# Optimization experiments

Measured on AMD Instinct MI355X. Metric: run time of the kernel, lower is better.

The kernel has to match this reference:

```python
import jax, jax.numpy as jnp
import numpy as np

N = 40000      # nodes
E = 640000     # edges
R = 4          # relations (n_edge_features)
F = 128        # n_node_features
H = 128        # n_hidden
NB = 2         # num_convolution_blocks
G = 64         # graphs in batch
OUT = 10       # n_output
MAXDEG = 10    # PyG MFConv default max_degree


def setup_inputs() -> dict:
    key = jax.random.key(0)
    ks = jax.random.split(key, 20)
    s = 0.05
    return {
        "x": jax.random.normal(ks[0], (N, F), dtype=jnp.float32),
        "edge_index": jax.random.randint(ks[1], (2, E), 0, N, dtype=jnp.int32),
        "edge_attr": jax.random.randint(ks[2], (E,), 0, R, dtype=jnp.int32),
        "batch_idx": jnp.sort(jax.random.randint(ks[3], (N,), 0, G, dtype=jnp.int32)),
        # node embedding Linear(F -> H)
        "W0": jax.random.normal(ks[4], (F, H), dtype=jnp.float32) * s,
        "b0": jnp.zeros((H,), dtype=jnp.float32),
        # per-block RGCNConv params (stacked over blocks)
        "rgcn_Wrel": jax.random.normal(ks[5], (NB, R, H, H), dtype=jnp.float32) * s,
        "rgcn_Wroot": jax.random.normal(ks[6], (NB, H, H), dtype=jnp.float32) * s,
        "rgcn_b": jnp.zeros((NB, H), dtype=jnp.float32),
        # per-block MFConv params: lins_l (bias) and lins_r (no bias), one per degree 0..MAXDEG
        "mf_Wl": jax.random.normal(ks[7], (NB, MAXDEG + 1, H, H), dtype=jnp.float32) * s,
        "mf_bl": jnp.zeros((NB, MAXDEG + 1, H), dtype=jnp.float32),
        "mf_Wr": jax.random.normal(ks[8], (NB, MAXDEG + 1, H, H), dtype=jnp.float32) * s,
        # after-pool MLP
        "W1": jax.random.normal(ks[9], (H, H), dtype=jnp.float32) * s,
        "b1": jnp.zeros((H,), dtype=jnp.float32),
        "W2": jax.random.normal(ks[10], (H, OUT), dtype=jnp.float32) * s,
        "b2": jnp.zeros((OUT,), dtype=jnp.float32),
    }


def _rgcn(h, Wrel, Wroot, b, src, dst, etype):
    # PyG RGCNConv: per-relation mean of neighbor features, then relation GEMM, plus root + bias
    n = h.shape[0]
    idx = dst * R + etype                                   # fused (node, relation) segment id
    msg = h[src]                                            # [E, H] gather
    sums = jax.ops.segment_sum(msg, idx, num_segments=n * R).reshape(n, R, -1)
    cnt = jax.ops.segment_sum(jnp.ones((msg.shape[0],), h.dtype), idx,
                              num_segments=n * R).reshape(n, R, 1)
    mean = jnp.where(cnt > 0, sums / jnp.maximum(cnt, 1.0), 0.0)
    return jnp.einsum('nrh,rho->no', mean, Wrel) + h @ Wroot + b


def _mfconv(h, Wl, bl, Wr, src, dst, deg):
    # PyG MFConv: sum-aggregate neighbors, then degree-specific lin_l(agg) + lin_r(x)
    n = h.shape[0]
    agg = jax.ops.segment_sum(h[src], dst, num_segments=n)  # [N, H]
    out = jnp.zeros((n, Wl.shape[-1]), h.dtype)
    for d in range(MAXDEG + 1):                             # small fixed loop over degree buckets
        m = (deg == d).astype(h.dtype)[:, None]
        out = out + m * (agg @ Wl[d] + bl[d] + h @ Wr[d])
    return out


def reference(x, edge_index, edge_attr, batch_idx,
              W0, b0, rgcn_Wrel, rgcn_Wroot, rgcn_b,
              mf_Wl, mf_bl, mf_Wr, W1, b1, W2, b2):
    src, dst = edge_index[0], edge_index[1]
    etype = edge_attr
    n = x.shape[0]
    # node degree at targets (all relations), clamped to MAXDEG (PyG MFConv)
    deg = jnp.clip(jax.ops.segment_sum(jnp.ones((src.shape[0],), jnp.int32), dst,
                                       num_segments=n), 0, MAXDEG)
    h = x @ W0 + b0
    for blk in range(NB):
        h = jax.nn.relu(h)
        h = _rgcn(h, rgcn_Wrel[blk], rgcn_Wroot[blk], rgcn_b[blk], src, dst, etype)
        h = jax.nn.relu(h)
        h = _mfconv(h, mf_Wl[blk], mf_bl[blk], mf_Wr[blk], src, dst, deg)
    pooled = jax.ops.segment_sum(h, batch_idx, num_segments=G)  # global add pool [G, H]
    out = jax.nn.relu(pooled @ W1 + b1) @ W2 + b2
    return out
```

## Files before the change

kernel.cpp:

```cpp
#include <hip/hip_runtime.h>
#include <hip/hip_bf16.h>

#define N_NODES 40000
#define N_EDGES 640000
#define R_REL 4
#define F_IN 128
#define H_DIM 128
#define NBLK 2
#define G_GRAPHS 64
#define N_OUT 10
#define MAXDEG 10
#define NSCAN_BLK ((N_NODES + 255) / 256)

typedef unsigned short u16;
typedef float f32x4 __attribute__((ext_vector_type(4)));
typedef short bf16x8 __attribute__((ext_vector_type(8)));

__device__ __forceinline__ float relu_f(float x){ return x > 0.f ? x : 0.f; }

__device__ __forceinline__ u16 f2bf(float f){
  union { float f; unsigned int u; } v; v.f = f;
  unsigned int r = v.u + 0x7fffu + ((v.u >> 16) & 1u);
  return (u16)(r >> 16);
}
__device__ __forceinline__ float b2f(u16 u){
  union { unsigned int u; float f; } v; v.u = ((unsigned int)u) << 16; return v.f;
}
__device__ __forceinline__ float blo(unsigned v){ return b2f((u16)v); }
__device__ __forceinline__ float bhi(unsigned v){ return b2f((u16)(v >> 16)); }

__device__ __forceinline__ void gload16(const void* g, void* l){
  __builtin_amdgcn_global_load_lds(
      (const __attribute__((address_space(1))) void*)g,
      (__attribute__((address_space(3))) void*)l, 16, 0, 0);
}

__device__ __forceinline__ void unpk8(uint4 v, float* f){
  f[0] = blo(v.x); f[1] = bhi(v.x);
  f[2] = blo(v.y); f[3] = bhi(v.y);
  f[4] = blo(v.z); f[5] = bhi(v.z);
  f[6] = blo(v.w); f[7] = bhi(v.w);
}

__global__ void k_cnt(const int* __restrict__ dst, const int* __restrict__ et, int* __restrict__ cnt4){
  int e = blockIdx.x * blockDim.x + threadIdx.x;
  if (e >= N_EDGES) return;
  atomicAdd(&cnt4[dst[e] * R_REL + et[e]], 1);
}

__global__ __launch_bounds__(256) void k_scan_a(const int* __restrict__ cnt4, int* __restrict__ deg,
                                                int* __restrict__ row_ptr, int* __restrict__ bsum,
                                                int* __restrict__ bhist){
  __shared__ int s[256];
  __shared__ int lh[16];
  int tid = threadIdx.x;
  int i = blockIdx.x * 256 + tid;
  if (tid < 16) lh[tid] = 0;
  int d = 0;
  if (i < N_NODES){
    int4 c = *(const int4*)(cnt4 + (size_t)i * 4);
    d = c.x + c.y + c.z + c.w;
    deg[i] = d;
  }
  s[tid] = d;
  __syncthreads();
  if (i < N_NODES){
    int dc = d > MAXDEG ? MAXDEG : d;
    atomicAdd(&lh[dc], 1);
  }
  for (int o = 1; o < 256; o <<= 1){
    int t = (tid >= o) ? s[tid - o] : 0;
    __syncthreads();
    s[tid] += t;
    __syncthreads();
  }
  if (i < N_NODES) row_ptr[i] = s[tid] - d;
  if (tid == 255) bsum[blockIdx.x] = s[255];
  if (tid <= MAXDEG) bhist[blockIdx.x * (MAXDEG + 1) + tid] = lh[tid];
}

__global__ __launch_bounds__(256) void k_scan_bb(int* __restrict__ bsum, int* __restrict__ bbase,
                                                 const int* __restrict__ bhist, int* __restrict__ pbase,
                                                 int* __restrict__ bcount, int* __restrict__ boff){
  __shared__ int s[256];
  __shared__ int cnt_s[MAXDEG + 1];
  __shared__ int off_s[MAXDEG + 1];
  int tid = threadIdx.x;
  int v = (tid < NSCAN_BLK) ? bsum[tid] : 0;
  s[tid] = v;
  __syncthreads();
  for (int o = 1; o < 256; o <<= 1){
    int t = (tid >= o) ? s[tid - o] : 0;
    __syncthreads();
    s[tid] += t;
    __syncthreads();
  }
  if (tid < NSCAN_BLK) bbase[tid] = s[tid] - v;

  if (tid <= MAXDEG){
    int run = 0;
    for (int b = 0; b < NSCAN_BLK; ++b){
      pbase[b * (MAXDEG + 1) + tid] = run;
      run += bhist[b * (MAXDEG + 1) + tid];
    }
    cnt_s[tid] = run;
    bcount[tid] = run;
  }
  __syncthreads();
  if (tid == 0){
    int acc = 0;
    for (int dd = 0; dd <= MAXDEG; ++dd){ off_s[dd] = acc; boff[dd] = acc; acc += cnt_s[dd]; }
  }
  __syncthreads();
  if (tid <= MAXDEG){
    int base = off_s[tid];
    for (int b = 0; b < NSCAN_BLK; ++b) pbase[b * (MAXDEG + 1) + tid] += base;
  }
}

__global__ __launch_bounds__(256) void k_scan_c(int* __restrict__ row_ptr, const int* __restrict__ bbase,
                                                const int* __restrict__ cnt4, int* __restrict__ rel_off,
                                                int* __restrict__ cursor){
  int i = blockIdx.x * 256 + threadIdx.x;
  if (i < N_NODES){
    int base = row_ptr[i] + bbase[blockIdx.x];
    row_ptr[i] = base;
    int4 c = *(const int4*)(cnt4 + (size_t)i * 4);
    int4 o;
    o.x = base;
    o.y = base + c.x;
    o.z = o.y + c.y;
    o.w = o.z + c.z;
    *(int4*)(rel_off + (size_t)i * 4) = o;
    *(int4*)(cursor + (size_t)i * 4) = o;
  }
  if (i == 0) row_ptr[N_NODES] = N_EDGES;
}

__global__ void k_csr_fill(const int* __restrict__ src, const int* __restrict__ dst,
                           const int* __restrict__ et,
                           int* __restrict__ cursor, int* __restrict__ esrc){
  int e = blockIdx.x * blockDim.x + threadIdx.x;
  if (e >= N_EDGES) return;
  int cell = dst[e] * R_REL + et[e];
  int p = atomicAdd(&cursor[cell], 1);
  esrc[p] = src[e];
}

__global__ __launch_bounds__(256) void k_bfill(const int* __restrict__ deg, const int* __restrict__ pbase,
                                               int* __restrict__ perm){
  __shared__ int lh[MAXDEG + 1];
  int tid = threadIdx.x;
  if (tid <= MAXDEG) lh[tid] = 0;
  __syncthreads();
  int i = blockIdx.x * 256 + tid;
  if (i < N_NODES){
    int d = deg[i]; if (d > MAXDEG) d = MAXDEG;
    int lpos = atomicAdd(&lh[d], 1);
    perm[pbase[blockIdx.x * (MAXDEG + 1) + d] + lpos] = i;
  }
}

__global__ __launch_bounds__(256) void k_cvtW_all(const float* __restrict__ s0, const float* __restrict__ s1,
                                                  const float* __restrict__ s2, const float* __restrict__ s3,
                                                  const float* __restrict__ s4,
                                                  u16* __restrict__ d0, u16* __restrict__ d1,
                                                  u16* __restrict__ d2, u16* __restrict__ d3,
                                                  u16* __restrict__ d4){
  __shared__ float s[32][33];
  int b = blockIdx.x;
  int m = b >> 4, tile = b & 15;
  const float* S; u16* D; int base;
  if (m < 1){ S = s0; D = d0; base = m; }
  else if (m < 9){ S = s1; D = d1; base = m - 1; }
  else if (m < 11){ S = s2; D = d2; base = m - 9; }
  else if (m < 33){ S = s3; D = d3; base = m - 11; }
  else { S = s4; D = d4; base = m - 33; }
  S += (size_t)base * 16384;
  D += (size_t)base * 16384;
  int tr = (tile >> 2) * 32, tc = (tile & 3) * 32;
  int c = threadIdx.x & 31, r0 = threadIdx.x >> 5;
  #pragma unroll
  for (int i = 0; i < 4; ++i){
    int r = r0 + i * 8;
    s[r][c] = S[(size_t)(tr + r) * 128 + tc + c];
  }
  __syncthreads();
  #pragma unroll
  for (int i = 0; i < 4; ++i){
    int r = r0 + i * 8;
    D[(size_t)(tc + r) * 128 + tr + c] = f2bf(s[c][r]);
  }
}

__global__ void k_cvtx(const float* __restrict__ x, u16* __restrict__ xb){
  int t = blockIdx.x * 256 + threadIdx.x;
  if (t >= (N_NODES * H_DIM) / 4) return;
  float4 v = ((const float4*)x)[t];
  uint2 o = make_uint2((unsigned)f2bf(v.x) | ((unsigned)f2bf(v.y) << 16),
                       (unsigned)f2bf(v.z) | ((unsigned)f2bf(v.w) << 16));
  ((uint2*)xb)[t] = o;
}

__global__ __launch_bounds__(256) void k_rgcn_agg(const u16* __restrict__ hb,
                                                  const int* __restrict__ rel_off,
                                                  const int* __restrict__ row_ptr,
                                                  const int* __restrict__ esrc,
                                                  u16* __restrict__ meanb){
  int node = blockIdx.x * 4 + (threadIdx.x >> 6);
  int lane = threadIdx.x & 63;
  int g = lane >> 4, c = lane & 15;
  int4 ro = *(const int4*)(rel_off + (size_t)node * 4);
  int nend = row_ptr[node + 1];
  int beg_g = (g == 0) ? ro.x : (g == 1) ? ro.y : (g == 2) ? ro.z : ro.w;
  int end_g = (g == 0) ? ro.y : (g == 1) ? ro.z : (g == 2) ? ro.w : nend;
  float acc[8];
  #pragma unroll
  for (int j = 0; j < 8; ++j) acc[j] = 0.f;
  const u16* hc = hb + c * 8;

  int e = beg_g;
  for (; e + 2 <= end_g; e += 2){
    int s0 = esrc[e], s1 = esrc[e + 1];
    uint4 v0 = *(const uint4*)(hc + (size_t)s0 * H_DIM);
    uint4 v1 = *(const uint4*)(hc + (size_t)s1 * H_DIM);
    float f0[8], f1[8];
    unpk8(v0, f0); unpk8(v1, f1);
    #pragma unroll
    for (int j = 0; j < 8; ++j) acc[j] += f0[j] + f1[j];
  }
  if (e < end_g){
    uint4 v0 = *(const uint4*)(hc + (size_t)esrc[e] * H_DIM);
    float f0[8];
    unpk8(v0, f0);
    #pragma unroll
    for (int j = 0; j < 8; ++j) acc[j] += f0[j];
  }
  int cnt = end_g - beg_g;
  float inv = cnt > 0 ? 1.f / (float)cnt : 0.f;
  unsigned p[4];
  #pragma unroll
  for (int q = 0; q < 4; ++q)
    p[q] = (unsigned)f2bf(acc[q * 2] * inv) | ((unsigned)f2bf(acc[q * 2 + 1] * inv) << 16);
  *(uint4*)(meanb + (size_t)node * R_REL * H_DIM + g * H_DIM + c * 8) =
      make_uint4(p[0], p[1], p[2], p[3]);
}

__global__ __launch_bounds__(256) void k_mf_agg(const u16* __restrict__ hb,
                                                const int* __restrict__ row_ptr,
                                                const int* __restrict__ esrc,
                                                u16* __restrict__ aggb){
  int node = blockIdx.x * 4 + (threadIdx.x >> 6);
  int lane = threadIdx.x & 63;
  int g = lane >> 4, c = lane & 15;
  int beg = row_ptr[node], end = row_ptr[node + 1];
  int T = end - beg;
  float acc[8];
  #pragma unroll
  for (int j = 0; j < 8; ++j) acc[j] = 0.f;
  const u16* hc = hb + c * 8;

  int i = 0;
  for (; i + 8 <= T; i += 8){
    int eA = beg + i + g, eB = beg + i + 4 + g;
    int sA = esrc[eA], sB = esrc[eB];
    uint4 vA = *(const uint4*)(hc + (size_t)sA * H_DIM);
    uint4 vB = *(const uint4*)(hc + (size_t)sB * H_DIM);
    float fA[8], fB[8];
    unpk8(vA, fA); unpk8(vB, fB);
    #pragma unroll
    for (int j = 0; j < 8; ++j) acc[j] += fA[j] + fB[j];
  }
  for (; i < T; i += 4){
    int e = beg + i + g;
    int ce = e < end ? e : end - 1;
    int s = esrc[ce];
    uint4 v = *(const uint4*)(hc + (size_t)s * H_DIM);
    float f[8];
    unpk8(v, f);
    float m = (e < end) ? 1.f : 0.f;
    #pragma unroll
    for (int j = 0; j < 8; ++j) acc[j] += f[j] * m;
  }
  #pragma unroll
  for (int j = 0; j < 8; ++j){
    acc[j] += __shfl_xor(acc[j], 16, 64);
    acc[j] += __shfl_xor(acc[j], 32, 64);
  }
  if (g == 0){
    unsigned p[4];
    #pragma unroll
    for (int q = 0; q < 4; ++q)
      p[q] = (unsigned)f2bf(acc[q * 2]) | ((unsigned)f2bf(acc[q * 2 + 1]) << 16);
    uint4 P = make_uint4(p[0], p[1], p[2], p[3]);
    *(uint4*)(aggb + (size_t)node * H_DIM + c * 8) = P;
  }
}


__global__ __launch_bounds__(512) void k_gemm0(const u16* __restrict__ xb, const u16* __restrict__ wt,
                                               const float* __restrict__ bias, u16* __restrict__ hbo){
  __shared__ u16 lds[32][128];
  int tid = threadIdx.x;
  int w = tid >> 6, lane = tid & 63;
  int m0 = blockIdx.x * 32;
  int rg = lane >> 4, cb = (lane & 15) << 4;
  int srow = w * 4 + rg;
  int swcb = cb ^ ((srow & 7) << 4);
  gload16(xb + (size_t)(m0 + srow) * F_IN + (swcb >> 1), &lds[w * 4][0]);
  __syncthreads();

  int arow = lane & 15, kg = lane >> 4;
  int col = w * 16 + arow;
  f32x4 acc[2];
  acc[0] = (f32x4){0.f, 0.f, 0.f, 0.f};
  acc[1] = (f32x4){0.f, 0.f, 0.f, 0.f};
  bf16x8 b[4];
  #pragma unroll
  for (int kk = 0; kk < 4; ++kk)
    b[kk] = *(const bf16x8*)(wt + (size_t)col * F_IN + kk * 32 + kg * 8);
  #pragma unroll
  for (int rt = 0; rt < 2; ++rt){
    int row = rt * 16 + arow;
    const char* base = (const char*)&lds[0][0] + row * 256;
    int sx = (row & 7) << 4;
    #pragma unroll
    for (int kk = 0; kk < 4; ++kk){
      bf16x8 a = *(const bf16x8*)(base + ((kk * 64 + kg * 16) ^ sx));
      acc[rt] = __builtin_amdgcn_mfma_f32_16x16x32_bf16(a, b[kk], acc[rt], 0, 0, 0);
    }
  }
  float bb = bias[col];
  #pragma unroll
  for (int rt = 0; rt < 2; ++rt)
    #pragma unroll
    for (int j = 0; j < 4; ++j){
      int gr = m0 + rt * 16 + kg * 4 + j;
      hbo[(size_t)gr * H_DIM + col] = f2bf(relu_f(acc[rt][j] + bb));
    }
}

__global__ __launch_bounds__(512) void k_rgcn_gemm(const u16* __restrict__ meanb, const u16* __restrict__ hb,
                                                   const u16* __restrict__ wrel, const u16* __restrict__ wroot,
                                                   const float* __restrict__ bias, u16* __restrict__ hbo){
  __shared__ u16 lds[5][32][128];
  int tid = threadIdx.x;
  int w = tid >> 6, lane = tid & 63;
  int m0 = blockIdx.x * 32;
  int rg = lane >> 4, cb = (lane & 15) << 4;
  int srow = w * 4 + rg;
  int swcb = cb ^ ((srow & 7) << 4);
  #pragma unroll
  for (int s = 0; s < 4; ++s)
    gload16(meanb + ((size_t)(m0 + srow) * R_REL + s) * H_DIM + (swcb >> 1), &lds[s][w * 4][0]);
  gload16(hb + (size_t)(m0 + srow) * H_DIM + (swcb >> 1), &lds[4][w * 4][0]);
  __syncthreads();

  int arow = lane & 15, kg = lane >> 4;
  int col = w * 16 + arow;
  f32x4 acc[2];
  acc[0] = (f32x4){0.f, 0.f, 0.f, 0.f};
  acc[1] = (f32x4){0.f, 0.f, 0.f, 0.f};
  #pragma unroll
  for (int s = 0; s < 5; ++s){
    const u16* WT = (s < 4) ? wrel + (size_t)s * 16384 : wroot;
    bf16x8 b[4];
    #pragma unroll
    for (int kk = 0; kk < 4; ++kk)
      b[kk] = *(const bf16x8*)(WT + (size_t)col * H_DIM + kk * 32 + kg * 8);
    #pragma unroll
    for (int rt = 0; rt < 2; ++rt){
      int row = rt * 16 + arow;
      const char* base = (const char*)&lds[s][0][0] + row * 256;
      int sx = (row & 7) << 4;
      #pragma unroll
      for (int kk = 0; kk < 4; ++kk){
        bf16x8 a = *(const bf16x8*)(base + ((kk * 64 + kg * 16) ^ sx));
        acc[rt] = __builtin_amdgcn_mfma_f32_16x16x32_bf16(a, b[kk], acc[rt], 0, 0, 0);
      }
    }
  }
  float bb = bias[col];
  #pragma unroll
  for (int rt = 0; rt < 2; ++rt)
    #pragma unroll
    for (int j = 0; j < 4; ++j){
      int gr = m0 + rt * 16 + kg * 4 + j;
      hbo[(size_t)gr * H_DIM + col] = f2bf(relu_f(acc[rt][j] + bb));
    }
}

template<int FINAL>
__global__ __launch_bounds__(512) void k_mf_gemm(const u16* __restrict__ aggb, const u16* __restrict__ hb,
                                                 const u16* __restrict__ wl, const u16* __restrict__ wr,
                                                 const float* __restrict__ bl,
                                                 const int* __restrict__ bcount, const int* __restrict__ boff,
                                                 const int* __restrict__ perm,
                                                 u16* __restrict__ hbo, float* __restrict__ hf){
  __shared__ u16 lds[2][32][128];
  __shared__ int rows_s[32];
  int t = blockIdx.x;
  int d = -1, tile = 0;
  for (int dd = 0; dd <= MAXDEG; ++dd){
    int nt = (bcount[dd] + 31) >> 5;
    if (t < nt){ d = dd; tile = t; break; }
    t -= nt;
  }
  if (d < 0) return;
  int cnt_d = bcount[d];
  int start = boff[d] + tile * 32;
  int nrows = cnt_d - tile * 32; if (nrows > 32) nrows = 32;

  int tid = threadIdx.x;
  int w = tid >> 6, lane = tid & 63;
  if (tid < 32) rows_s[tid] = (tid < nrows) ? perm[start + tid] : -1;

  int rg = lane >> 4, cb = (lane & 15) << 4;
  int srow = w * 4 + rg;
  int swcb = cb ^ ((srow & 7) << 4);
  int node = perm[start + (srow < nrows ? srow : 0)];
  gload16(aggb + (size_t)node * H_DIM + (swcb >> 1), &lds[0][w * 4][0]);
  gload16(hb   + (size_t)node * H_DIM + (swcb >> 1), &lds[1][w * 4][0]);
  __syncthreads();

  int arow = lane & 15, kg = lane >> 4;
  int col = w * 16 + arow;
  f32x4 acc[2];
  acc[0] = (f32x4){0.f, 0.f, 0.f, 0.f};
  acc[1] = (f32x4){0.f, 0.f, 0.f, 0.f};
  #pragma unroll
  for (int s = 0; s < 2; ++s){
    const u16* WT = (s ? wr : wl) + (size_t)d * 16384;
    bf16x8 b[4];
    #pragma unroll
    for (int kk = 0; kk < 4; ++kk)
      b[kk] = *(const bf16x8*)(WT + (size_t)col * H_DIM + kk * 32 + kg * 8);
    #pragma unroll
    for (int rt = 0; rt < 2; ++rt){
      int row = rt * 16 + arow;
      const char* base = (const char*)&lds[s][0][0] + row * 256;
      int sx = (row & 7) << 4;
      #pragma unroll
      for (int kk = 0; kk < 4; ++kk){
        bf16x8 a = *(const bf16x8*)(base + ((kk * 64 + kg * 16) ^ sx));
        acc[rt] = __builtin_amdgcn_mfma_f32_16x16x32_bf16(a, b[kk], acc[rt], 0, 0, 0);
      }
    }
  }
  float bb = bl[(size_t)d * H_DIM + col];
  #pragma unroll
  for (int rt = 0; rt < 2; ++rt)
    #pragma unroll
    for (int j = 0; j < 4; ++j){
      int gr = rows_s[rt * 16 + kg * 4 + j];
      if (gr >= 0){
        float v = acc[rt][j] + bb;
        if (FINAL) hf[(size_t)gr * H_DIM + col] = v;
        else       hbo[(size_t)gr * H_DIM + col] = f2bf(relu_f(v));
      }
    }
}

__global__ void k_goff(const int* __restrict__ batch, int* __restrict__ goff){
  int n = blockIdx.x * blockDim.x + threadIdx.x;
  if (n >= N_NODES) return;
  int b = batch[n];
  int bp = (n == 0) ? -1 : batch[n - 1];
  for (int g = bp + 1; g <= b; ++g) goff[g] = n;
  if (n == N_NODES - 1){
    for (int g = b + 1; g <= G_GRAPHS; ++g) goff[g] = N_NODES;
  }
}

__global__ __launch_bounds__(256) void k_pool(const float* __restrict__ h, const int* __restrict__ goff,
                                              float* __restrict__ pooled){
  __shared__ float4 sred[8][32];
  int g = blockIdx.x;
  int tid = threadIdx.x;
  int rg = tid >> 5, lane = tid & 31;
  int beg = goff[g], end = goff[g + 1];
  float4 acc = make_float4(0.f, 0.f, 0.f, 0.f);
  for (int n = beg + rg; n < end; n += 8){
    float4 v = ((const float4*)(h + (size_t)n * H_DIM))[lane];
    acc.x += v.x; acc.y += v.y; acc.z += v.z; acc.w += v.w;
  }
  sred[rg][lane] = acc;
  __syncthreads();
  if (tid < 32){
    float4 s = sred[0][tid];
    #pragma unroll
    for (int r = 1; r < 8; ++r){
      float4 v = sred[r][tid];
      s.x += v.x; s.y += v.y; s.z += v.z; s.w += v.w;
    }
    *(float4*)(pooled + (size_t)g * H_DIM + tid * 4) = s;
  }
}

__global__ __launch_bounds__(128) void k_mlp(const float* __restrict__ pooled,
                                             const float* __restrict__ W1, const float* __restrict__ b1,
                                             const float* __restrict__ W2, const float* __restrict__ b2,
                                             float* __restrict__ out){
  __shared__ float Ts[128];
  int g = blockIdx.x, j = threadIdx.x;
  const float* p = pooled + (size_t)g * H_DIM;
  float s = b1[j];
  for (int k = 0; k < H_DIM; ++k) s += p[k] * W1[k * H_DIM + j];
  Ts[j] = relu_f(s);
  __syncthreads();
  if (j < N_OUT){
    float o = b2[j];
    for (int k = 0; k < H_DIM; ++k) o += Ts[k] * W2[k * N_OUT + j];
    out[(size_t)g * N_OUT + j] = o;
  }
}

extern "C" void kernel_launch(void* const* d_in, const int* in_sizes, int n_in,
                              void* d_out, int out_size, void* d_ws, size_t ws_size,
                              hipStream_t stream){
  const float* x      = (const float*)d_in[0];
  const int*   ei     = (const int*)d_in[1];
  const int*   ea     = (const int*)d_in[2];
  const int*   batch  = (const int*)d_in[3];
  const float* W0     = (const float*)d_in[4];
  const float* b0     = (const float*)d_in[5];
  const float* rWrel  = (const float*)d_in[6];
  const float* rWroot = (const float*)d_in[7];
  const float* rb     = (const float*)d_in[8];
  const float* mWl    = (const float*)d_in[9];
  const float* mbl    = (const float*)d_in[10];
  const float* mWr    = (const float*)d_in[11];
  const float* W1     = (const float*)d_in[12];
  const float* b1     = (const float*)d_in[13];
  const float* W2     = (const float*)d_in[14];
  const float* b2     = (const float*)d_in[15];
  float* out = (float*)d_out;

  const int* src = ei;
  const int* dst = ei + N_EDGES;

  char* ws = (char*)d_ws;
  size_t off = 0;
  auto alloc = [&](size_t bytes) -> void* {
    void* p = ws + off;
    off += (bytes + 255) & ~(size_t)255;
    return p;
  };
  u16* xb      = (u16*)alloc((size_t)N_NODES * H_DIM * 2);
  u16* hbA     = (u16*)alloc((size_t)N_NODES * H_DIM * 2);
  u16* hbB     = (u16*)alloc((size_t)N_NODES * H_DIM * 2);
  u16* meanb   = (u16*)alloc((size_t)N_NODES * R_REL * H_DIM * 2);
  u16* aggb    = meanb;
  float* hf    = (float*)alloc((size_t)N_NODES * H_DIM * 4);
  u16* wt0     = (u16*)alloc((size_t)1 * 16384 * 2);
  u16* wtRel   = (u16*)alloc((size_t)NBLK * R_REL * 16384 * 2);
  u16* wtRoot  = (u16*)alloc((size_t)NBLK * 16384 * 2);
  u16* wtWl    = (u16*)alloc((size_t)NBLK * (MAXDEG + 1) * 16384 * 2);
  u16* wtWr    = (u16*)alloc((size_t)NBLK * (MAXDEG + 1) * 16384 * 2);
  float* pooled = (float*)alloc((size_t)G_GRAPHS * H_DIM * 4);
  int* cnt4     = (int*)alloc((size_t)N_NODES * R_REL * 4);
  int* deg      = (int*)alloc((size_t)N_NODES * 4);
  int* row_ptr  = (int*)alloc((size_t)(N_NODES + 1) * 4);
  int* rel_off  = (int*)alloc((size_t)N_NODES * R_REL * 4);
  int* cursor   = (int*)alloc((size_t)N_NODES * R_REL * 4);
  int* esrc     = (int*)alloc((size_t)N_EDGES * 4);
  int* bsum     = (int*)alloc((size_t)NSCAN_BLK * 4);
  int* bbase    = (int*)alloc((size_t)NSCAN_BLK * 4);
  int* bhist    = (int*)alloc((size_t)NSCAN_BLK * (MAXDEG + 1) * 4);
  int* pbase    = (int*)alloc((size_t)NSCAN_BLK * (MAXDEG + 1) * 4);
  int* perm     = (int*)alloc((size_t)N_NODES * 4);
  int* bcount   = (int*)alloc(16 * 4);
  int* boff     = (int*)alloc(16 * 4);
  int* goff     = (int*)alloc((size_t)(G_GRAPHS + 1) * 4);

  hipMemsetAsync(cnt4, 0, (size_t)N_NODES * R_REL * 4, stream);

  k_cnt<<<(N_EDGES + 255) / 256, 256, 0, stream>>>(dst, ea, cnt4);
  k_scan_a<<<NSCAN_BLK, 256, 0, stream>>>(cnt4, deg, row_ptr, bsum, bhist);
  k_scan_bb<<<1, 256, 0, stream>>>(bsum, bbase, bhist, pbase, bcount, boff);
  k_scan_c<<<NSCAN_BLK, 256, 0, stream>>>(row_ptr, bbase, cnt4, rel_off, cursor);
  k_csr_fill<<<(N_EDGES + 255) / 256, 256, 0, stream>>>(src, dst, ea, cursor, esrc);
  k_bfill<<<NSCAN_BLK, 256, 0, stream>>>(deg, pbase, perm);
  k_goff<<<(N_NODES + 255) / 256, 256, 0, stream>>>(batch, goff);

  k_cvtW_all<<<55 * 16, 256, 0, stream>>>(W0, rWrel, rWroot, mWl, mWr,
                                          wt0, wtRel, wtRoot, wtWl, wtWr);
  k_cvtx<<<(N_NODES * H_DIM / 4 + 255) / 256, 256, 0, stream>>>(x, xb);

  k_gemm0<<<N_NODES / 32, 512, 0, stream>>>(xb, wt0, b0, hbA);

  u16* hin = hbA;
  u16* hout = hbB;
  for (int blk = 0; blk < NBLK; ++blk){
    k_rgcn_agg<<<N_NODES / 4, 256, 0, stream>>>(hin, rel_off, row_ptr, esrc, meanb);
    k_rgcn_gemm<<<N_NODES / 32, 512, 0, stream>>>(meanb, hin,
        wtRel + (size_t)blk * R_REL * 16384,
        wtRoot + (size_t)blk * 16384,
        rb + (size_t)blk * H_DIM, hout);
    { u16* tmp = hin; hin = hout; hout = tmp; }

    k_mf_agg<<<N_NODES / 4, 256, 0, stream>>>(hin, row_ptr, esrc, aggb);
    const u16* wl_b = wtWl + (size_t)blk * (MAXDEG + 1) * 16384;
    const u16* wr_b = wtWr + (size_t)blk * (MAXDEG + 1) * 16384;
    const float* bl_b = mbl + (size_t)blk * (MAXDEG + 1) * H_DIM;
    int grid_mf = N_NODES / 32 + MAXDEG + 1;
    if (blk == NBLK - 1)
      k_mf_gemm<1><<<grid_mf, 512, 0, stream>>>(aggb, hin, wl_b, wr_b, bl_b,
                                                bcount, boff, perm, hout, hf);
    else
      k_mf_gemm<0><<<grid_mf, 512, 0, stream>>>(aggb, hin, wl_b, wr_b, bl_b,
                                                bcount, boff, perm, hout, hf);
    { u16* tmp = hin; hin = hout; hout = tmp; }
  }

  k_pool<<<G_GRAPHS, 256, 0, stream>>>(hf, goff, pooled);
  k_mlp<<<G_GRAPHS, 128, 0, stream>>>(pooled, W1, b1, W2, b2, out);
}
```

Baseline: 359.3 us.

## Fuse x conversion into gemm0, merge goff/bfill and pool/mlp, unroll rgcn gather

```diff
diff --git a/kernel.cpp b/kernel.cpp
--- a/kernel.cpp
+++ b/kernel.cpp
@@ -147,8 +147,9 @@
   esrc[p] = src[e];
 }
 
-__global__ __launch_bounds__(256) void k_bfill(const int* __restrict__ deg, const int* __restrict__ pbase,
-                                               int* __restrict__ perm){
+__global__ __launch_bounds__(256) void k_bfill_goff(const int* __restrict__ deg, const int* __restrict__ pbase,
+                                                    int* __restrict__ perm,
+                                                    const int* __restrict__ batch, int* __restrict__ goff){
   __shared__ int lh[MAXDEG + 1];
   int tid = threadIdx.x;
   if (tid <= MAXDEG) lh[tid] = 0;
@@ -158,6 +159,13 @@
     int d = deg[i]; if (d > MAXDEG) d = MAXDEG;
     int lpos = atomicAdd(&lh[d], 1);
     perm[pbase[blockIdx.x * (MAXDEG + 1) + d] + lpos] = i;
+
+    int b = batch[i];
+    int bp = (i == 0) ? -1 : batch[i - 1];
+    for (int g = bp + 1; g <= b; ++g) goff[g] = i;
+    if (i == N_NODES - 1){
+      for (int g = b + 1; g <= G_GRAPHS; ++g) goff[g] = N_NODES;
+    }
   }
 }
 
@@ -193,15 +201,6 @@
   }
 }
 
-__global__ void k_cvtx(const float* __restrict__ x, u16* __restrict__ xb){
-  int t = blockIdx.x * 256 + threadIdx.x;
-  if (t >= (N_NODES * H_DIM) / 4) return;
-  float4 v = ((const float4*)x)[t];
-  uint2 o = make_uint2((unsigned)f2bf(v.x) | ((unsigned)f2bf(v.y) << 16),
-                       (unsigned)f2bf(v.z) | ((unsigned)f2bf(v.w) << 16));
-  ((uint2*)xb)[t] = o;
-}
-
 __global__ __launch_bounds__(256) void k_rgcn_agg(const u16* __restrict__ hb,
                                                   const int* __restrict__ rel_off,
                                                   const int* __restrict__ row_ptr,
@@ -220,6 +219,17 @@
   const u16* hc = hb + c * 8;
 
   int e = beg_g;
+  for (; e + 4 <= end_g; e += 4){
+    int s0 = esrc[e], s1 = esrc[e + 1], s2 = esrc[e + 2], s3 = esrc[e + 3];
+    uint4 v0 = *(const uint4*)(hc + (size_t)s0 * H_DIM);
+    uint4 v1 = *(const uint4*)(hc + (size_t)s1 * H_DIM);
+    uint4 v2 = *(const uint4*)(hc + (size_t)s2 * H_DIM);
+    uint4 v3 = *(const uint4*)(hc + (size_t)s3 * H_DIM);
+    float f0[8], f1[8], f2[8], f3[8];
+    unpk8(v0, f0); unpk8(v1, f1); unpk8(v2, f2); unpk8(v3, f3);
+    #pragma unroll
+    for (int j = 0; j < 8; ++j) acc[j] += (f0[j] + f1[j]) + (f2[j] + f3[j]);
+  }
   for (; e + 2 <= end_g; e += 2){
     int s0 = esrc[e], s1 = esrc[e + 1];
     uint4 v0 = *(const uint4*)(hc + (size_t)s0 * H_DIM);
@@ -298,16 +308,25 @@
 }
 
 
-__global__ __launch_bounds__(512) void k_gemm0(const u16* __restrict__ xb, const u16* __restrict__ wt,
+__global__ __launch_bounds__(512) void k_gemm0(const float* __restrict__ x, const u16* __restrict__ wt,
                                                const float* __restrict__ bias, u16* __restrict__ hbo){
   __shared__ u16 lds[32][128];
   int tid = threadIdx.x;
   int w = tid >> 6, lane = tid & 63;
   int m0 = blockIdx.x * 32;
-  int rg = lane >> 4, cb = (lane & 15) << 4;
-  int srow = w * 4 + rg;
-  int swcb = cb ^ ((srow & 7) << 4);
-  gload16(xb + (size_t)(m0 + srow) * F_IN + (swcb >> 1), &lds[w * 4][0]);
+  {
+    int rg = lane >> 4, cb = (lane & 15) << 4;
+    int srow = w * 4 + rg;
+    int swcb = cb ^ ((srow & 7) << 4);
+    const float* xs = x + (size_t)(m0 + srow) * F_IN + (swcb >> 1);
+    float4 u = *(const float4*)xs;
+    float4 v = *(const float4*)(xs + 4);
+    unsigned p0 = (unsigned)f2bf(u.x) | ((unsigned)f2bf(u.y) << 16);
+    unsigned p1 = (unsigned)f2bf(u.z) | ((unsigned)f2bf(u.w) << 16);
+    unsigned p2 = (unsigned)f2bf(v.x) | ((unsigned)f2bf(v.y) << 16);
+    unsigned p3 = (unsigned)f2bf(v.z) | ((unsigned)f2bf(v.w) << 16);
+    *(uint4*)((char*)&lds[0][0] + w * 1024 + lane * 16) = make_uint4(p0, p1, p2, p3);
+  }
   __syncthreads();
 
   int arow = lane & 15, kg = lane >> 4;
@@ -461,20 +480,13 @@
     }
 }
 
-__global__ void k_goff(const int* __restrict__ batch, int* __restrict__ goff){
-  int n = blockIdx.x * blockDim.x + threadIdx.x;
-  if (n >= N_NODES) return;
-  int b = batch[n];
-  int bp = (n == 0) ? -1 : batch[n - 1];
-  for (int g = bp + 1; g <= b; ++g) goff[g] = n;
-  if (n == N_NODES - 1){
-    for (int g = b + 1; g <= G_GRAPHS; ++g) goff[g] = N_NODES;
-  }
-}
-
-__global__ __launch_bounds__(256) void k_pool(const float* __restrict__ h, const int* __restrict__ goff,
-                                              float* __restrict__ pooled){
+__global__ __launch_bounds__(256) void k_poolmlp(const float* __restrict__ h, const int* __restrict__ goff,
+                                                 const float* __restrict__ W1, const float* __restrict__ b1,
+                                                 const float* __restrict__ W2, const float* __restrict__ b2,
+                                                 float* __restrict__ out){
   __shared__ float4 sred[8][32];
+  __shared__ float pv[128];
+  __shared__ float Ts[128];
   int g = blockIdx.x;
   int tid = threadIdx.x;
   int rg = tid >> 5, lane = tid & 31;
@@ -493,25 +505,19 @@
       float4 v = sred[r][tid];
       s.x += v.x; s.y += v.y; s.z += v.z; s.w += v.w;
     }
-    *(float4*)(pooled + (size_t)g * H_DIM + tid * 4) = s;
-  }
-}
-
-__global__ __launch_bounds__(128) void k_mlp(const float* __restrict__ pooled,
-                                             const float* __restrict__ W1, const float* __restrict__ b1,
-                                             const float* __restrict__ W2, const float* __restrict__ b2,
-                                             float* __restrict__ out){
-  __shared__ float Ts[128];
-  int g = blockIdx.x, j = threadIdx.x;
-  const float* p = pooled + (size_t)g * H_DIM;
-  float s = b1[j];
-  for (int k = 0; k < H_DIM; ++k) s += p[k] * W1[k * H_DIM + j];
-  Ts[j] = relu_f(s);
-  __syncthreads();
-  if (j < N_OUT){
-    float o = b2[j];
-    for (int k = 0; k < H_DIM; ++k) o += Ts[k] * W2[k * N_OUT + j];
-    out[(size_t)g * N_OUT + j] = o;
+    *(float4*)&pv[tid * 4] = s;
+  }
+  __syncthreads();
+  if (tid < 128){
+    float s = b1[tid];
+    for (int k = 0; k < H_DIM; ++k) s += pv[k] * W1[k * H_DIM + tid];
+    Ts[tid] = relu_f(s);
+  }
+  __syncthreads();
+  if (tid < N_OUT){
+    float o = b2[tid];
+    for (int k = 0; k < H_DIM; ++k) o += Ts[k] * W2[k * N_OUT + tid];
+    out[(size_t)g * N_OUT + tid] = o;
   }
 }
 
@@ -546,7 +552,6 @@
     off += (bytes + 255) & ~(size_t)255;
     return p;
   };
-  u16* xb      = (u16*)alloc((size_t)N_NODES * H_DIM * 2);
   u16* hbA     = (u16*)alloc((size_t)N_NODES * H_DIM * 2);
   u16* hbB     = (u16*)alloc((size_t)N_NODES * H_DIM * 2);
   u16* meanb   = (u16*)alloc((size_t)N_NODES * R_REL * H_DIM * 2);
@@ -557,7 +562,6 @@
   u16* wtRoot  = (u16*)alloc((size_t)NBLK * 16384 * 2);
   u16* wtWl    = (u16*)alloc((size_t)NBLK * (MAXDEG + 1) * 16384 * 2);
   u16* wtWr    = (u16*)alloc((size_t)NBLK * (MAXDEG + 1) * 16384 * 2);
-  float* pooled = (float*)alloc((size_t)G_GRAPHS * H_DIM * 4);
   int* cnt4     = (int*)alloc((size_t)N_NODES * R_REL * 4);
   int* deg      = (int*)alloc((size_t)N_NODES * 4);
   int* row_ptr  = (int*)alloc((size_t)(N_NODES + 1) * 4);
@@ -580,14 +584,12 @@
   k_scan_bb<<<1, 256, 0, stream>>>(bsum, bbase, bhist, pbase, bcount, boff);
   k_scan_c<<<NSCAN_BLK, 256, 0, stream>>>(row_ptr, bbase, cnt4, rel_off, cursor);
   k_csr_fill<<<(N_EDGES + 255) / 256, 256, 0, stream>>>(src, dst, ea, cursor, esrc);
-  k_bfill<<<NSCAN_BLK, 256, 0, stream>>>(deg, pbase, perm);
-  k_goff<<<(N_NODES + 255) / 256, 256, 0, stream>>>(batch, goff);
+  k_bfill_goff<<<NSCAN_BLK, 256, 0, stream>>>(deg, pbase, perm, batch, goff);
 
   k_cvtW_all<<<55 * 16, 256, 0, stream>>>(W0, rWrel, rWroot, mWl, mWr,
                                           wt0, wtRel, wtRoot, wtWl, wtWr);
-  k_cvtx<<<(N_NODES * H_DIM / 4 + 255) / 256, 256, 0, stream>>>(x, xb);
-
-  k_gemm0<<<N_NODES / 32, 512, 0, stream>>>(xb, wt0, b0, hbA);
+
+  k_gemm0<<<N_NODES / 32, 512, 0, stream>>>(x, wt0, b0, hbA);
 
   u16* hin = hbA;
   u16* hout = hbB;
@@ -613,6 +615,5 @@
     { u16* tmp = hin; hin = hout; hout = tmp; }
   }
 
-  k_pool<<<G_GRAPHS, 256, 0, stream>>>(hf, goff, pooled);
-  k_mlp<<<G_GRAPHS, 128, 0, stream>>>(pooled, W1, b1, W2, b2, out);
-}
+  k_poolmlp<<<G_GRAPHS, 256, 0, stream>>>(hf, goff, W1, b1, W2, b2, out);
+}
```

Result: faster. 345.9 us (-3.7%).
